# Performance work log

Measured on AMD Instinct MI355X. Metric: run time of the kernel, lower is better.

Reference implementation:

```python
import jax, jax.numpy as jnp
import numpy as np

N = 150000   # nodes
E = 150000   # edges per edge type
D = 128      # n_map
T = 10       # edge types: pre0-3, suc0-3, left, right
L = 4        # fuse layers
VOCAB = 16   # mark_type_dim
EPS = 1e-5


def _mlp(x, W1, b1, W2, b2):
    # MLPLayer(in, hid, out): Linear -> ReLU -> Linear
    return jax.nn.relu(x @ W1.T + b1) @ W2.T + b2


def setup_inputs() -> dict:
    key = jax.random.key(0)
    ks = iter(jax.random.split(key, 40))
    s = 0.02
    f = lambda shape: (jax.random.normal(next(ks), shape, dtype=jnp.float32) * s)
    inp = {
        'ctrs': jax.random.normal(next(ks), (N, 2), dtype=jnp.float32),
        'feats': jax.random.normal(next(ks), (N, 2), dtype=jnp.float32),
        # input MLP (2 -> D -> D)
        'in_W1': f((D, 2)), 'in_b1': f((D,)), 'in_W2': f((D, D)), 'in_b2': f((D,)),
        # seg MLP (2 -> D -> D)
        'seg_W1': f((D, 2)), 'seg_b1': f((D,)), 'seg_W2': f((D, D)), 'seg_b2': f((D,)),
        # mark embedding and meta MLP (2D -> D -> D)
        'embed': f((VOCAB, D)),
        'meta_W1': f((D, 2 * D)), 'meta_b1': f((D,)), 'meta_W2': f((D, D)), 'meta_b2': f((D,)),
        # fuse weights stacked over L layers
        'ctr_W': f((L, D, D)),            # Linear no bias
        'edge_W': f((L, T, D, D)),        # per-edge-type Linear no bias
        'norm_g': jnp.ones((L, D), jnp.float32),
        'norm_b': jnp.zeros((L, D), jnp.float32),
        'ctr2_W1': f((L, D, D)), 'ctr2_b1': f((L, D)),
        'ctr2_W2': f((L, D, D)), 'ctr2_b2': f((L, D)),
        # integer graph structure
        'mark_type': jax.random.randint(next(ks), (N,), 0, VOCAB, dtype=jnp.int32),
        'edge_u': jax.random.randint(next(ks), (T, E), 0, N, dtype=jnp.int32),
        'edge_v': jax.random.randint(next(ks), (T, E), 0, N, dtype=jnp.int32),
    }
    return inp


def reference(ctrs, feats, in_W1, in_b1, in_W2, in_b2,
              seg_W1, seg_b1, seg_W2, seg_b2,
              embed, meta_W1, meta_b1, meta_W2, meta_b2,
              ctr_W, edge_W, norm_g, norm_b,
              ctr2_W1, ctr2_b1, ctr2_W2, ctr2_b2,
              mark_type, edge_u, edge_v):
    feat = jax.nn.relu(_mlp(ctrs, in_W1, in_b1, in_W2, in_b2)
                       + _mlp(feats, seg_W1, seg_b1, seg_W2, seg_b2))  # [N, D]
    res = feat
    for i in range(L):
        temp = feat @ ctr_W[i].T
        for t in range(T):  # gather -> small GEMM -> scatter-add per edge type
            msg = feat[edge_v[t]] @ edge_W[i, t].T        # [E, D]
            temp = temp.at[edge_u[t]].add(msg)
        # GroupNorm(1, D) on [N, D]: normalize over channels per node
        mu = jnp.mean(temp, axis=-1, keepdims=True)
        var = jnp.var(temp, axis=-1, keepdims=True)
        feat = (temp - mu) * jax.lax.rsqrt(var + EPS) * norm_g[i] + norm_b[i]
        feat = jax.nn.relu(feat)
        feat = _mlp(feat, ctr2_W1[i], ctr2_b1[i], ctr2_W2[i], ctr2_b2[i])
        feat = jax.nn.relu(feat + res)
        res = feat
    meta = embed[mark_type]                               # [N, D]
    feat = _mlp(jnp.concatenate([feat, meta], axis=1), meta_W1, meta_b1, meta_W2, meta_b2)
    return feat
```

## Files before the change

### kernel.cpp

```cpp
#include <hip/hip_runtime.h>

#define D 128
#define NT 10
#define NL 4
#define BN 128
#define SCH 1024

typedef __attribute__((ext_vector_type(8))) short bf16x8;
typedef __attribute__((ext_vector_type(4))) float f32x4;

__device__ inline unsigned short f2bf(float x) {
    union { float f; unsigned u; } v; v.f = x;
    unsigned r = v.u + 0x7FFFu + ((v.u >> 16) & 1u);
    return (unsigned short)(r >> 16);
}
__device__ inline float bf2f(unsigned short h) {
    union { unsigned u; float f; } v; v.u = ((unsigned)h) << 16;
    return v.f;
}

__global__ void input_hidden_kernel(const float* __restrict__ ctrs,
                                    const float* __restrict__ feats,
                                    const float* __restrict__ inW1,
                                    const float* __restrict__ inb1,
                                    const float* __restrict__ segW1,
                                    const float* __restrict__ segb1,
                                    float* __restrict__ h_in,
                                    float* __restrict__ h_seg, int N) {
    int gid = blockIdx.x * blockDim.x + threadIdx.x;
    int n = gid >> 5;
    int c = gid & 31;
    if (n >= N) return;
    float x0 = ctrs[2 * n], x1 = ctrs[2 * n + 1];
    float y0 = feats[2 * n], y1 = feats[2 * n + 1];
    int o0 = c * 4;
    float hi[4], hs[4];
#pragma unroll
    for (int j = 0; j < 4; ++j) {
        int o = o0 + j;
        float a = fmaf(x0, inW1[2 * o], fmaf(x1, inW1[2 * o + 1], inb1[o]));
        hi[j] = fmaxf(a, 0.f);
        float b = fmaf(y0, segW1[2 * o], fmaf(y1, segW1[2 * o + 1], segb1[o]));
        hs[j] = fmaxf(b, 0.f);
    }
    *(float4*)&h_in[(size_t)n * D + o0] = make_float4(hi[0], hi[1], hi[2], hi[3]);
    *(float4*)&h_seg[(size_t)n * D + o0] = make_float4(hs[0], hs[1], hs[2], hs[3]);
}

template <int BIAS, int RELU, int ADDIN>
__global__ __launch_bounds__(256) void gemm_mfma_kernel(
    const float* __restrict__ A, const float* __restrict__ W,
    const float* __restrict__ bias, const float* addin, float* out, int N,
    int ldw) {
    __shared__ unsigned short a_hi[128][40], a_lo[128][40];
    __shared__ unsigned short w_hi[128][40], w_lo[128][40];
    int t = threadIdx.x;
    int wave = t >> 6, lane = t & 63;
    int fr = lane & 15, fq = lane >> 4;
    int n0 = blockIdx.x * BN;
    f32x4 acc[2][8];
#pragma unroll
    for (int m = 0; m < 2; ++m)
#pragma unroll
        for (int n = 0; n < 8; ++n) acc[m][n] = (f32x4){0.f, 0.f, 0.f, 0.f};

    for (int kc = 0; kc < 4; ++kc) {
        int k0 = kc * 32;
#pragma unroll
        for (int i = 0; i < 4; ++i) {
            int idx = i * 256 + t;
            int row = idx >> 3, c4 = idx & 7;
            int n = n0 + row;
            float4 v = make_float4(0.f, 0.f, 0.f, 0.f);
            if (n < N) v = *(const float4*)&A[(size_t)n * D + k0 + c4 * 4];
            ushort4 h, l;
            h.x = f2bf(v.x); l.x = f2bf(v.x - bf2f(h.x));
            h.y = f2bf(v.y); l.y = f2bf(v.y - bf2f(h.y));
            h.z = f2bf(v.z); l.z = f2bf(v.z - bf2f(h.z));
            h.w = f2bf(v.w); l.w = f2bf(v.w - bf2f(h.w));
            *(ushort4*)&a_hi[row][c4 * 4] = h;
            *(ushort4*)&a_lo[row][c4 * 4] = l;
        }
#pragma unroll
        for (int i = 0; i < 4; ++i) {
            int idx = i * 256 + t;
            int row = idx >> 3, c4 = idx & 7;
            float4 v = *(const float4*)&W[(size_t)row * ldw + k0 + c4 * 4];
            ushort4 h, l;
            h.x = f2bf(v.x); l.x = f2bf(v.x - bf2f(h.x));
            h.y = f2bf(v.y); l.y = f2bf(v.y - bf2f(h.y));
            h.z = f2bf(v.z); l.z = f2bf(v.z - bf2f(h.z));
            h.w = f2bf(v.w); l.w = f2bf(v.w - bf2f(h.w));
            *(ushort4*)&w_hi[row][c4 * 4] = h;
            *(ushort4*)&w_lo[row][c4 * 4] = l;
        }
        __syncthreads();

        bf16x8 ah[2], al[2];
#pragma unroll
        for (int m = 0; m < 2; ++m) {
            int row = wave * 32 + m * 16 + fr;
            ah[m] = *(const bf16x8*)&a_hi[row][fq * 8];
            al[m] = *(const bf16x8*)&a_lo[row][fq * 8];
        }
#pragma unroll
        for (int n = 0; n < 8; ++n) {
            int wr = n * 16 + fr;
            bf16x8 wh = *(const bf16x8*)&w_hi[wr][fq * 8];
            bf16x8 wl = *(const bf16x8*)&w_lo[wr][fq * 8];
#pragma unroll
            for (int m = 0; m < 2; ++m) {
                acc[m][n] = __builtin_amdgcn_mfma_f32_16x16x32_bf16(
                    ah[m], wh, acc[m][n], 0, 0, 0);
                acc[m][n] = __builtin_amdgcn_mfma_f32_16x16x32_bf16(
                    ah[m], wl, acc[m][n], 0, 0, 0);
                acc[m][n] = __builtin_amdgcn_mfma_f32_16x16x32_bf16(
                    al[m], wh, acc[m][n], 0, 0, 0);
            }
        }
        __syncthreads();
    }
#pragma unroll
    for (int m = 0; m < 2; ++m) {
#pragma unroll
        for (int j = 0; j < 4; ++j) {
            int row = n0 + wave * 32 + m * 16 + fq * 4 + j;
            if (row < N) {
#pragma unroll
                for (int n = 0; n < 8; ++n) {
                    int col = n * 16 + fr;
                    float r = acc[m][n][j];
                    if (BIAS) r += bias[col];
                    if (ADDIN) r += addin[(size_t)row * D + col];
                    if (RELU) r = fmaxf(r, 0.f);
                    out[(size_t)row * D + col] = r;
                }
            }
        }
    }
}

__global__ void csr_hist_kernel(const int* __restrict__ edge_u, int* deg,
                                int N, int E) {
    int gid = blockIdx.x * blockDim.x + threadIdx.x;
    if (gid >= NT * E) return;
    int t = gid / E;
    int u = edge_u[gid];
    atomicAdd(&deg[(size_t)t * N + u], 1);
}

__global__ __launch_bounds__(256) void csr_chunksum_kernel(
    const int* __restrict__ deg, int* csum, int N, int nch) {
    int b = blockIdx.x;
    int t = b / nch, ch = b % nch;
    int tid = threadIdx.x;
    const int* dg = deg + (size_t)t * N;
    int base = ch * SCH + tid * 4;
    int s = 0;
#pragma unroll
    for (int j = 0; j < 4; ++j) {
        int idx = base + j;
        if (idx < N) s += dg[idx];
    }
#pragma unroll
    for (int off = 32; off; off >>= 1) s += __shfl_down(s, off);
    __shared__ int wsum[4];
    if ((tid & 63) == 0) wsum[tid >> 6] = s;
    __syncthreads();
    if (tid == 0) csum[b] = wsum[0] + wsum[1] + wsum[2] + wsum[3];
}

__global__ void csr_chunkscan_kernel(int* csum, int* rowptr, int N, int nch) {
    int t = threadIdx.x;
    if (t >= NT) return;
    int run = 0;
    for (int i = 0; i < nch; ++i) {
        int v = csum[t * nch + i];
        csum[t * nch + i] = run;
        run += v;
    }
    rowptr[(size_t)t * (N + 1) + N] = run;
}

__global__ __launch_bounds__(256) void csr_blockscan_kernel(
    const int* __restrict__ deg, const int* __restrict__ csum, int* rowptr,
    int* cur, int N, int nch) {
    int b = blockIdx.x;
    int t = b / nch, ch = b % nch;
    int tid = threadIdx.x;
    const int* dg = deg + (size_t)t * N;
    int base = ch * SCH + tid * 4;
    int d[4];
    int s = 0;
#pragma unroll
    for (int j = 0; j < 4; ++j) {
        int idx = base + j;
        d[j] = (idx < N) ? dg[idx] : 0;
        s += d[j];
    }
    __shared__ int ps[256];
    ps[tid] = s;
    __syncthreads();
    for (int off = 1; off < 256; off <<= 1) {
        int v = (tid >= off) ? ps[tid - off] : 0;
        __syncthreads();
        ps[tid] += v;
        __syncthreads();
    }
    int excl = (tid ? ps[tid - 1] : 0) + csum[b];
    size_t rb = (size_t)t * (N + 1);
#pragma unroll
    for (int j = 0; j < 4; ++j) {
        int idx = base + j;
        if (idx < N) {
            rowptr[rb + idx] = excl;
            cur[rb + idx] = excl;
            excl += d[j];
        }
    }
}

__global__ void csr_fill_kernel(const int* __restrict__ edge_u,
                                const int* __restrict__ edge_v, int* cur,
                                int* col, int N, int E) {
    int gid = blockIdx.x * blockDim.x + threadIdx.x;
    if (gid >= NT * E) return;
    int t = gid / E;
    int u = edge_u[gid];
    int v = edge_v[gid];
    int pos = atomicAdd(&cur[(size_t)t * (N + 1) + u], 1);
    col[(size_t)t * E + pos] = v;
}

template <int NORM>
__global__ __launch_bounds__(256) void csr_gather_multi_kernel(
    const float* __restrict__ Y, const int* __restrict__ rowptr,
    const int* __restrict__ col, float* temp, int N, int nt, size_t strideY,
    int E, const float* __restrict__ g, const float* __restrict__ b) {
    int wid = (int)((blockIdx.x * (size_t)blockDim.x + threadIdx.x) >> 6);
    int lane = threadIdx.x & 63;
    if (wid >= N) return;
    size_t ro = (size_t)wid * D + lane * 2;
    float2 acc = *(float2*)&temp[ro];
    for (int j = 0; j < nt; ++j) {
        const int* rp = rowptr + (size_t)j * (N + 1);
        int beg = rp[wid];
        int end = rp[wid + 1];
        const float* Yj = Y + (size_t)j * strideY;
        const int* cj = col + (size_t)j * E;
        for (int k = beg; k < end; ++k) {
            int v = cj[k];
            float2 y = *(const float2*)&Yj[(size_t)v * D + lane * 2];
            acc.x += y.x;
            acc.y += y.y;
        }
    }
    if (NORM) {
        float s = acc.x + acc.y;
        float sq = acc.x * acc.x + acc.y * acc.y;
#pragma unroll
        for (int off = 32; off; off >>= 1) {
            s += __shfl_xor(s, off);
            sq += __shfl_xor(sq, off);
        }
        float mu = s * (1.f / 128.f);
        float var = sq * (1.f / 128.f) - mu * mu;
        float rs = rsqrtf(var + 1e-5f);
        acc.x = fmaxf(fmaf((acc.x - mu) * rs, g[lane * 2], b[lane * 2]), 0.f);
        acc.y = fmaxf(fmaf((acc.y - mu) * rs, g[lane * 2 + 1], b[lane * 2 + 1]), 0.f);
    }
    *(float2*)&temp[ro] = acc;
}

__global__ __launch_bounds__(256) void norm_relu_kernel(float* temp,
                                                        const float* __restrict__ g,
                                                        const float* __restrict__ b,
                                                        int N) {
    int wid = (int)((blockIdx.x * (size_t)blockDim.x + threadIdx.x) >> 6);
    int lane = threadIdx.x & 63;
    if (wid >= N) return;
    float2 x = *(float2*)&temp[(size_t)wid * D + lane * 2];
    float s = x.x + x.y;
    float sq = x.x * x.x + x.y * x.y;
#pragma unroll
    for (int off = 32; off; off >>= 1) {
        s += __shfl_xor(s, off);
        sq += __shfl_xor(sq, off);
    }
    float mu = s * (1.f / 128.f);
    float var = sq * (1.f / 128.f) - mu * mu;
    float rs = rsqrtf(var + 1e-5f);
    float r0 = fmaxf(fmaf((x.x - mu) * rs, g[lane * 2], b[lane * 2]), 0.f);
    float r1 = fmaxf(fmaf((x.y - mu) * rs, g[lane * 2 + 1], b[lane * 2 + 1]), 0.f);
    *(float2*)&temp[(size_t)wid * D + lane * 2] = make_float2(r0, r1);
}

__global__ void gather_meta_kernel(const int* __restrict__ mark,
                                   const float* __restrict__ embed, float* out,
                                   int N) {
    int gid = blockIdx.x * blockDim.x + threadIdx.x;
    int n = gid >> 5;
    int c = gid & 31;
    if (n >= N) return;
    *(float4*)&out[(size_t)n * D + c * 4] =
        *(const float4*)&embed[(size_t)mark[n] * D + c * 4];
}

static inline void launch_gemm(const float* A, const float* W, const float* bias,
                               const float* addin, float* out, int N, int ldw,
                               bool relu, hipStream_t s) {
    dim3 grid((N + BN - 1) / BN), blk(256);
    bool B = bias != nullptr, AD = addin != nullptr;
    if (B && !relu && !AD)
        gemm_mfma_kernel<1, 0, 0><<<grid, blk, 0, s>>>(A, W, bias, addin, out, N, ldw);
    else if (B && relu && AD)
        gemm_mfma_kernel<1, 1, 1><<<grid, blk, 0, s>>>(A, W, bias, addin, out, N, ldw);
    else if (!B && !relu && !AD)
        gemm_mfma_kernel<0, 0, 0><<<grid, blk, 0, s>>>(A, W, bias, addin, out, N, ldw);
    else if (B && relu && !AD)
        gemm_mfma_kernel<1, 1, 0><<<grid, blk, 0, s>>>(A, W, bias, addin, out, N, ldw);
    else if (!B && relu && AD)
        gemm_mfma_kernel<0, 1, 1><<<grid, blk, 0, s>>>(A, W, bias, addin, out, N, ldw);
    else if (!B && relu && !AD)
        gemm_mfma_kernel<0, 1, 0><<<grid, blk, 0, s>>>(A, W, bias, addin, out, N, ldw);
    else if (!B && !relu && AD)
        gemm_mfma_kernel<0, 0, 1><<<grid, blk, 0, s>>>(A, W, bias, addin, out, N, ldw);
    else
        gemm_mfma_kernel<1, 0, 1><<<grid, blk, 0, s>>>(A, W, bias, addin, out, N, ldw);
}

extern "C" void kernel_launch(void* const* d_in, const int* in_sizes, int n_in,
                              void* d_out, int out_size, void* d_ws,
                              size_t ws_size, hipStream_t stream) {
    const float* ctrs = (const float*)d_in[0];
    const float* feats = (const float*)d_in[1];
    const float* in_W1 = (const float*)d_in[2];
    const float* in_b1 = (const float*)d_in[3];
    const float* in_W2 = (const float*)d_in[4];
    const float* in_b2 = (const float*)d_in[5];
    const float* seg_W1 = (const float*)d_in[6];
    const float* seg_b1 = (const float*)d_in[7];
    const float* seg_W2 = (const float*)d_in[8];
    const float* seg_b2 = (const float*)d_in[9];
    const float* embed = (const float*)d_in[10];
    const float* meta_W1 = (const float*)d_in[11];
    const float* meta_b1 = (const float*)d_in[12];
    const float* meta_W2 = (const float*)d_in[13];
    const float* meta_b2 = (const float*)d_in[14];
    const float* ctr_W = (const float*)d_in[15];
    const float* edge_W = (const float*)d_in[16];
    const float* norm_g = (const float*)d_in[17];
    const float* norm_b = (const float*)d_in[18];
    const float* ctr2_W1 = (const float*)d_in[19];
    const float* ctr2_b1 = (const float*)d_in[20];
    const float* ctr2_W2 = (const float*)d_in[21];
    const float* ctr2_b2 = (const float*)d_in[22];
    const int* mark_type = (const int*)d_in[23];
    const int* edge_u = (const int*)d_in[24];
    const int* edge_v = (const int*)d_in[25];

    const int N = in_sizes[0] / 2;
    const int E = in_sizes[24] / NT;
    const size_t ND = (size_t)N * D;
    const int nch = (N + SCH - 1) / SCH;

    float* F = (float*)d_ws;
    float* T1 = (float*)d_ws + ND;
    float* SC = (float*)d_out;

    int* rowptr = (int*)((float*)d_ws + 2 * ND);
    int* col = rowptr + (size_t)NT * (N + 1);
    size_t base_ws = (2 * ND) * sizeof(float) +
                     ((size_t)NT * (N + 1) + (size_t)NT * E) * sizeof(int);
    size_t out_need = ((size_t)NT * N + (size_t)NT * (N + 1) +
                       2 * (size_t)NT * nch) * sizeof(int);
    bool use_csr = (ws_size >= base_ws) &&
                   ((size_t)out_size * sizeof(float) >= out_need);

    float* Yws = (float*)((char*)d_ws + ((base_ws + 255) & ~(size_t)255));
    int slots = 0;
    if (use_csr && ws_size > base_ws + 256)
        slots = (int)((ws_size - base_ws - 256) / (ND * sizeof(float)));
    if (slots > NT) slots = NT;

    dim3 blk(256);
    dim3 g32((N * 32 + 255) / 256);
    dim3 g64(((size_t)N * 64 + 255) / 256);
    dim3 gTE(((size_t)NT * E + 255) / 256);

    if (use_csr) {
        int* deg = (int*)d_out;
        int* cur = deg + (size_t)NT * N;
        int* csum = cur + (size_t)NT * (N + 1);
        hipMemsetAsync(deg, 0, (size_t)NT * N * sizeof(int), stream);
        csr_hist_kernel<<<gTE, blk, 0, stream>>>(edge_u, deg, N, E);
        csr_chunksum_kernel<<<NT * nch, blk, 0, stream>>>(deg, csum, N, nch);
        csr_chunkscan_kernel<<<1, 64, 0, stream>>>(csum, rowptr, N, nch);
        csr_blockscan_kernel<<<NT * nch, blk, 0, stream>>>(deg, csum, rowptr,
                                                           cur, N, nch);
        csr_fill_kernel<<<gTE, blk, 0, stream>>>(edge_u, edge_v, cur, col, N, E);
    }

    input_hidden_kernel<<<g32, blk, 0, stream>>>(ctrs, feats, in_W1, in_b1,
                                                 seg_W1, seg_b1, T1, SC, N);
    launch_gemm(T1, in_W2, in_b2, nullptr, F, N, D, false, stream);
    launch_gemm(SC, seg_W2, seg_b2, F, F, N, D, true, stream);

    for (int i = 0; i < NL; ++i) {
        launch_gemm(F, ctr_W + (size_t)i * D * D, nullptr, nullptr, T1, N, D,
                    false, stream);
        if (use_csr && slots >= 1) {
            int ngroups = (NT + slots - 1) / slots;
            for (int g0 = 0, grp = 0; g0 < NT; g0 += slots, ++grp) {
                int nt = (NT - g0 < slots) ? (NT - g0) : slots;
                for (int j = 0; j < nt; ++j)
                    launch_gemm(F, edge_W + ((size_t)i * NT + g0 + j) * D * D,
                                nullptr, nullptr, Yws + (size_t)j * ND, N, D,
                                false, stream);
                bool last = (grp == ngroups - 1);
                if (last && ngroups == 1)
                    csr_gather_multi_kernel<1><<<g64, blk, 0, stream>>>(
                        Yws, rowptr + (size_t)g0 * (N + 1), col + (size_t)g0 * E,
                        T1, N, nt, ND, E, norm_g + (size_t)i * D,
                        norm_b + (size_t)i * D);
                else
                    csr_gather_multi_kernel<0><<<g64, blk, 0, stream>>>(
                        Yws, rowptr + (size_t)g0 * (N + 1), col + (size_t)g0 * E,
                        T1, N, nt, ND, E, nullptr, nullptr);
            }
            if (ngroups > 1)
                norm_relu_kernel<<<g64, blk, 0, stream>>>(
                    T1, norm_g + (size_t)i * D, norm_b + (size_t)i * D, N);
        } else {
            for (int t = 0; t < NT; ++t) {
                launch_gemm(F, edge_W + ((size_t)i * NT + t) * D * D, nullptr,
                            nullptr, SC, N, D, false, stream);
                csr_gather_multi_kernel<0><<<g64, blk, 0, stream>>>(
                    SC, rowptr + (size_t)t * (N + 1), col + (size_t)t * E, T1,
                    N, 1, 0, E, nullptr, nullptr);
            }
            norm_relu_kernel<<<g64, blk, 0, stream>>>(
                T1, norm_g + (size_t)i * D, norm_b + (size_t)i * D, N);
        }
        launch_gemm(T1, ctr2_W1 + (size_t)i * D * D, ctr2_b1 + (size_t)i * D,
                    nullptr, SC, N, D, true, stream);
        launch_gemm(SC, ctr2_W2 + (size_t)i * D * D, ctr2_b2 + (size_t)i * D, F,
                    F, N, D, true, stream);
    }

    gather_meta_kernel<<<g32, blk, 0, stream>>>(mark_type, embed, SC, N);
    launch_gemm(F, meta_W1, meta_b1, nullptr, T1, N, 2 * D, false, stream);
    launch_gemm(SC, meta_W1 + D, nullptr, T1, T1, N, 2 * D, true, stream);
    launch_gemm(T1, meta_W2, meta_b2, nullptr, (float*)d_out, N, D, false,
                stream);
}
```

Before: 4.722 ms.

## Preconvert weights to split bf16 once and stream multi-output GEMM over activation tile

Adds a one-time kernel that converts all 57 weight matrices to hi/lo bf16 pairs, so the GEMMs no longer redo that conversion per block. The GEMM now loads activations straight from global memory into registers with no LDS staging or barriers, and it can loop over up to 11 weight matrices per row tile. This lets one launch produce the ctr_W result and all ten edge-type results while reusing the A fragments. It also reorganises workspace buffers and drops the separate norm kernel. The cost is that weight fragments come uncached-in-LDS from global/L2 and register pressure rises.

```diff
diff --git a/kernel.cpp b/kernel.cpp
--- a/kernel.cpp
+++ b/kernel.cpp
@@ -3,11 +3,15 @@
 #define D 128
 #define NT 10
 #define NL 4
-#define BN 128
 #define SCH 1024
+#define NMAT 57
+#define MATSZ 32768
 
 typedef __attribute__((ext_vector_type(8))) short bf16x8;
 typedef __attribute__((ext_vector_type(4))) float f32x4;
+
+struct OutPtrs { float* p[11]; };
+struct CvtTab { const float* src[NMAT]; int ldw[NMAT]; };
 
 __device__ inline unsigned short f2bf(float x) {
     union { float f; unsigned u; } v; v.f = x;
@@ -17,6 +21,36 @@
 __device__ inline float bf2f(unsigned short h) {
     union { unsigned u; float f; } v; v.u = ((unsigned)h) << 16;
     return v.f;
+}
+
+__device__ inline void cvt8(const float4& v0, const float4& v1, bf16x8& h,
+                            bf16x8& l) {
+    float f[8] = {v0.x, v0.y, v0.z, v0.w, v1.x, v1.y, v1.z, v1.w};
+#pragma unroll
+    for (int j = 0; j < 8; ++j) {
+        unsigned short hh = f2bf(f[j]);
+        h[j] = (short)hh;
+        l[j] = (short)f2bf(f[j] - bf2f(hh));
+    }
+}
+
+__global__ __launch_bounds__(256) void wcvt_kernel(CvtTab tab,
+                                                   unsigned short* dst) {
+    int bid = blockIdx.x;
+    int mat = bid >> 4;
+    if (mat >= NMAT) return;
+    int e = (bid & 15) * 1024 + threadIdx.x * 4;
+    int o = e >> 7, k = e & 127;
+    const float* s = tab.src[mat];
+    int ldw = tab.ldw[mat];
+    float4 v = *(const float4*)&s[(size_t)o * ldw + k];
+    ushort4 h, l;
+    h.x = f2bf(v.x); l.x = f2bf(v.x - bf2f(h.x));
+    h.y = f2bf(v.y); l.y = f2bf(v.y - bf2f(h.y));
+    h.z = f2bf(v.z); l.z = f2bf(v.z - bf2f(h.z));
+    h.w = f2bf(v.w); l.w = f2bf(v.w - bf2f(h.w));
+    *(ushort4*)&dst[(size_t)mat * MATSZ + e] = h;
+    *(ushort4*)&dst[(size_t)mat * MATSZ + 16384 + e] = l;
 }
 
 __global__ void input_hidden_kernel(const float* __restrict__ ctrs,
@@ -48,92 +82,74 @@
 }
 
 template <int BIAS, int RELU, int ADDIN>
-__global__ __launch_bounds__(256) void gemm_mfma_kernel(
-    const float* __restrict__ A, const float* __restrict__ W,
-    const float* __restrict__ bias, const float* addin, float* out, int N,
-    int ldw) {
-    __shared__ unsigned short a_hi[128][40], a_lo[128][40];
-    __shared__ unsigned short w_hi[128][40], w_lo[128][40];
+__global__ __launch_bounds__(256) void gemm_stream_kernel(
+    const float* __restrict__ A, const unsigned short* __restrict__ Wc,
+    int nw, OutPtrs outs, const float* __restrict__ bias,
+    const float* __restrict__ addin, int N) {
     int t = threadIdx.x;
     int wave = t >> 6, lane = t & 63;
     int fr = lane & 15, fq = lane >> 4;
-    int n0 = blockIdx.x * BN;
-    f32x4 acc[2][8];
-#pragma unroll
-    for (int m = 0; m < 2; ++m)
-#pragma unroll
-        for (int n = 0; n < 8; ++n) acc[m][n] = (f32x4){0.f, 0.f, 0.f, 0.f};
-
-    for (int kc = 0; kc < 4; ++kc) {
-        int k0 = kc * 32;
-#pragma unroll
-        for (int i = 0; i < 4; ++i) {
-            int idx = i * 256 + t;
-            int row = idx >> 3, c4 = idx & 7;
-            int n = n0 + row;
-            float4 v = make_float4(0.f, 0.f, 0.f, 0.f);
-            if (n < N) v = *(const float4*)&A[(size_t)n * D + k0 + c4 * 4];
-            ushort4 h, l;
-            h.x = f2bf(v.x); l.x = f2bf(v.x - bf2f(h.x));
-            h.y = f2bf(v.y); l.y = f2bf(v.y - bf2f(h.y));
-            h.z = f2bf(v.z); l.z = f2bf(v.z - bf2f(h.z));
-            h.w = f2bf(v.w); l.w = f2bf(v.w - bf2f(h.w));
-            *(ushort4*)&a_hi[row][c4 * 4] = h;
-            *(ushort4*)&a_lo[row][c4 * 4] = l;
-        }
-#pragma unroll
-        for (int i = 0; i < 4; ++i) {
-            int idx = i * 256 + t;
-            int row = idx >> 3, c4 = idx & 7;
-            float4 v = *(const float4*)&W[(size_t)row * ldw + k0 + c4 * 4];
-            ushort4 h, l;
-            h.x = f2bf(v.x); l.x = f2bf(v.x - bf2f(h.x));
-            h.y = f2bf(v.y); l.y = f2bf(v.y - bf2f(h.y));
-            h.z = f2bf(v.z); l.z = f2bf(v.z - bf2f(h.z));
-            h.w = f2bf(v.w); l.w = f2bf(v.w - bf2f(h.w));
-            *(ushort4*)&w_hi[row][c4 * 4] = h;
-            *(ushort4*)&w_lo[row][c4 * 4] = l;
-        }
-        __syncthreads();
-
-        bf16x8 ah[2], al[2];
+    int rbase = blockIdx.x * 128 + wave * 32;
+    int r0 = rbase + fr, r1 = rbase + 16 + fr;
+    bool ok0 = r0 < N, ok1 = r1 < N;
+    const float* a0 = A + (size_t)r0 * D;
+    const float* a1 = A + (size_t)r1 * D;
+
+    for (int w = 0; w < nw; ++w) {
+        const unsigned short* wm = Wc + (size_t)w * MATSZ;
+        f32x4 acc[2][8];
+#pragma unroll
+        for (int m = 0; m < 2; ++m)
+#pragma unroll
+            for (int n = 0; n < 8; ++n) acc[m][n] = (f32x4){0.f, 0.f, 0.f, 0.f};
+
+#pragma unroll
+        for (int kc = 0; kc < 4; ++kc) {
+            int ko = kc * 32 + fq * 8;
+            bf16x8 ah0, al0, ah1, al1;
+            {
+                float4 v0 = {0.f, 0.f, 0.f, 0.f}, v1 = {0.f, 0.f, 0.f, 0.f};
+                if (ok0) {
+                    v0 = *(const float4*)(a0 + ko);
+                    v1 = *(const float4*)(a0 + ko + 4);
+                }
+                cvt8(v0, v1, ah0, al0);
+                float4 u0 = {0.f, 0.f, 0.f, 0.f}, u1 = {0.f, 0.f, 0.f, 0.f};
+                if (ok1) {
+                    u0 = *(const float4*)(a1 + ko);
+                    u1 = *(const float4*)(a1 + ko + 4);
+                }
+                cvt8(u0, u1, ah1, al1);
+            }
+#pragma unroll
+            for (int n = 0; n < 8; ++n) {
+                const unsigned short* wp = wm + (size_t)(n * 16 + fr) * D + ko;
+                bf16x8 wh = *(const bf16x8*)wp;
+                bf16x8 wl = *(const bf16x8*)(wp + 16384);
+                acc[0][n] = __builtin_amdgcn_mfma_f32_16x16x32_bf16(ah0, wh, acc[0][n], 0, 0, 0);
+                acc[0][n] = __builtin_amdgcn_mfma_f32_16x16x32_bf16(ah0, wl, acc[0][n], 0, 0, 0);
+                acc[0][n] = __builtin_amdgcn_mfma_f32_16x16x32_bf16(al0, wh, acc[0][n], 0, 0, 0);
+                acc[1][n] = __builtin_amdgcn_mfma_f32_16x16x32_bf16(ah1, wh, acc[1][n], 0, 0, 0);
+                acc[1][n] = __builtin_amdgcn_mfma_f32_16x16x32_bf16(ah1, wl, acc[1][n], 0, 0, 0);
+                acc[1][n] = __builtin_amdgcn_mfma_f32_16x16x32_bf16(al1, wh, acc[1][n], 0, 0, 0);
+            }
+        }
+        float* outp = outs.p[w];
 #pragma unroll
         for (int m = 0; m < 2; ++m) {
-            int row = wave * 32 + m * 16 + fr;
-            ah[m] = *(const bf16x8*)&a_hi[row][fq * 8];
-            al[m] = *(const bf16x8*)&a_lo[row][fq * 8];
-        }
-#pragma unroll
-        for (int n = 0; n < 8; ++n) {
-            int wr = n * 16 + fr;
-            bf16x8 wh = *(const bf16x8*)&w_hi[wr][fq * 8];
-            bf16x8 wl = *(const bf16x8*)&w_lo[wr][fq * 8];
-#pragma unroll
-            for (int m = 0; m < 2; ++m) {
-                acc[m][n] = __builtin_amdgcn_mfma_f32_16x16x32_bf16(
-                    ah[m], wh, acc[m][n], 0, 0, 0);
-                acc[m][n] = __builtin_amdgcn_mfma_f32_16x16x32_bf16(
-                    ah[m], wl, acc[m][n], 0, 0, 0);
-                acc[m][n] = __builtin_amdgcn_mfma_f32_16x16x32_bf16(
-                    al[m], wh, acc[m][n], 0, 0, 0);
-            }
-        }
-        __syncthreads();
-    }
-#pragma unroll
-    for (int m = 0; m < 2; ++m) {
-#pragma unroll
-        for (int j = 0; j < 4; ++j) {
-            int row = n0 + wave * 32 + m * 16 + fq * 4 + j;
-            if (row < N) {
-#pragma unroll
-                for (int n = 0; n < 8; ++n) {
-                    int col = n * 16 + fr;
-                    float r = acc[m][n][j];
-                    if (BIAS) r += bias[col];
-                    if (ADDIN) r += addin[(size_t)row * D + col];
-                    if (RELU) r = fmaxf(r, 0.f);
-                    out[(size_t)row * D + col] = r;
+#pragma unroll
+            for (int j = 0; j < 4; ++j) {
+                int row = rbase + m * 16 + fq * 4 + j;
+                if (row < N) {
+#pragma unroll
+                    for (int n = 0; n < 8; ++n) {
+                        int colx = n * 16 + fr;
+                        float r = acc[m][n][j];
+                        if (BIAS) r += bias[colx];
+                        if (ADDIN) r += addin[(size_t)row * D + colx];
+                        if (RELU) r = fmaxf(r, 0.f);
+                        outp[(size_t)row * D + colx] = r;
+                    }
                 }
             }
         }
@@ -272,29 +288,6 @@
     *(float2*)&temp[ro] = acc;
 }
 
-__global__ __launch_bounds__(256) void norm_relu_kernel(float* temp,
-                                                        const float* __restrict__ g,
-                                                        const float* __restrict__ b,
-                                                        int N) {
-    int wid = (int)((blockIdx.x * (size_t)blockDim.x + threadIdx.x) >> 6);
-    int lane = threadIdx.x & 63;
-    if (wid >= N) return;
-    float2 x = *(float2*)&temp[(size_t)wid * D + lane * 2];
-    float s = x.x + x.y;
-    float sq = x.x * x.x + x.y * x.y;
-#pragma unroll
-    for (int off = 32; off; off >>= 1) {
-        s += __shfl_xor(s, off);
-        sq += __shfl_xor(sq, off);
-    }
-    float mu = s * (1.f / 128.f);
-    float var = sq * (1.f / 128.f) - mu * mu;
-    float rs = rsqrtf(var + 1e-5f);
-    float r0 = fmaxf(fmaf((x.x - mu) * rs, g[lane * 2], b[lane * 2]), 0.f);
-    float r1 = fmaxf(fmaf((x.y - mu) * rs, g[lane * 2 + 1], b[lane * 2 + 1]), 0.f);
-    *(float2*)&temp[(size_t)wid * D + lane * 2] = make_float2(r0, r1);
-}
-
 __global__ void gather_meta_kernel(const int* __restrict__ mark,
                                    const float* __restrict__ embed, float* out,
                                    int N) {
@@ -306,27 +299,29 @@
         *(const float4*)&embed[(size_t)mark[n] * D + c * 4];
 }
 
-static inline void launch_gemm(const float* A, const float* W, const float* bias,
-                               const float* addin, float* out, int N, int ldw,
-                               bool relu, hipStream_t s) {
-    dim3 grid((N + BN - 1) / BN), blk(256);
+static inline void launch_gemm1(const float* A, const unsigned short* Wc,
+                                const float* bias, const float* addin,
+                                float* out, int N, bool relu, hipStream_t s) {
+    OutPtrs o{};
+    o.p[0] = out;
+    dim3 grid((N + 127) / 128), blk(256);
     bool B = bias != nullptr, AD = addin != nullptr;
     if (B && !relu && !AD)
-        gemm_mfma_kernel<1, 0, 0><<<grid, blk, 0, s>>>(A, W, bias, addin, out, N, ldw);
+        gemm_stream_kernel<1, 0, 0><<<grid, blk, 0, s>>>(A, Wc, 1, o, bias, addin, N);
     else if (B && relu && AD)
-        gemm_mfma_kernel<1, 1, 1><<<grid, blk, 0, s>>>(A, W, bias, addin, out, N, ldw);
-    else if (!B && !relu && !AD)
-        gemm_mfma_kernel<0, 0, 0><<<grid, blk, 0, s>>>(A, W, bias, addin, out, N, ldw);
+        gemm_stream_kernel<1, 1, 1><<<grid, blk, 0, s>>>(A, Wc, 1, o, bias, addin, N);
     else if (B && relu && !AD)
-        gemm_mfma_kernel<1, 1, 0><<<grid, blk, 0, s>>>(A, W, bias, addin, out, N, ldw);
+        gemm_stream_kernel<1, 1, 0><<<grid, blk, 0, s>>>(A, Wc, 1, o, bias, addin, N);
+    else if (B && !relu && AD)
+        gemm_stream_kernel<1, 0, 1><<<grid, blk, 0, s>>>(A, Wc, 1, o, bias, addin, N);
     else if (!B && relu && AD)
-        gemm_mfma_kernel<0, 1, 1><<<grid, blk, 0, s>>>(A, W, bias, addin, out, N, ldw);
+        gemm_stream_kernel<0, 1, 1><<<grid, blk, 0, s>>>(A, Wc, 1, o, bias, addin, N);
     else if (!B && relu && !AD)
-        gemm_mfma_kernel<0, 1, 0><<<grid, blk, 0, s>>>(A, W, bias, addin, out, N, ldw);
+        gemm_stream_kernel<0, 1, 0><<<grid, blk, 0, s>>>(A, Wc, 1, o, bias, addin, N);
     else if (!B && !relu && AD)
-        gemm_mfma_kernel<0, 0, 1><<<grid, blk, 0, s>>>(A, W, bias, addin, out, N, ldw);
+        gemm_stream_kernel<0, 0, 1><<<grid, blk, 0, s>>>(A, Wc, 1, o, bias, addin, N);
     else
-        gemm_mfma_kernel<1, 0, 1><<<grid, blk, 0, s>>>(A, W, bias, addin, out, N, ldw);
+        gemm_stream_kernel<0, 0, 0><<<grid, blk, 0, s>>>(A, Wc, 1, o, bias, addin, N);
 }
 
 extern "C" void kernel_launch(void* const* d_in, const int* in_sizes, int n_in,
@@ -364,31 +359,47 @@
     const size_t ND = (size_t)N * D;
     const int nch = (N + SCH - 1) / SCH;
 
-    float* F = (float*)d_ws;
-    float* T1 = (float*)d_ws + ND;
+    unsigned short* Wcvt = (unsigned short*)d_ws;
+    size_t wcB = ((size_t)NMAT * MATSZ * sizeof(unsigned short) + 255) & ~(size_t)255;
+    float* F = (float*)((char*)d_ws + wcB);
+    int* rowptr = (int*)(F + ND);
+    int* col = rowptr + (size_t)NT * (N + 1);
+    size_t used = (size_t)((char*)(col + (size_t)NT * E) - (char*)d_ws);
+    used = (used + 255) & ~(size_t)255;
+    float* Yws = (float*)((char*)d_ws + used);
+    long navail = 0;
+    if (ws_size > used) navail = (long)((ws_size - used) / (ND * sizeof(float)));
+    if (navail > 11) navail = 11;
+    if (navail < 1) navail = 1;
+
     float* SC = (float*)d_out;
 
-    int* rowptr = (int*)((float*)d_ws + 2 * ND);
-    int* col = rowptr + (size_t)NT * (N + 1);
-    size_t base_ws = (2 * ND) * sizeof(float) +
-                     ((size_t)NT * (N + 1) + (size_t)NT * E) * sizeof(int);
-    size_t out_need = ((size_t)NT * N + (size_t)NT * (N + 1) +
-                       2 * (size_t)NT * nch) * sizeof(int);
-    bool use_csr = (ws_size >= base_ws) &&
-                   ((size_t)out_size * sizeof(float) >= out_need);
-
-    float* Yws = (float*)((char*)d_ws + ((base_ws + 255) & ~(size_t)255));
-    int slots = 0;
-    if (use_csr && ws_size > base_ws + 256)
-        slots = (int)((ws_size - base_ws - 256) / (ND * sizeof(float)));
-    if (slots > NT) slots = NT;
+    CvtTab tab;
+    tab.src[0] = in_W2;  tab.ldw[0] = D;
+    tab.src[1] = seg_W2; tab.ldw[1] = D;
+    for (int i = 0; i < NL; ++i) { tab.src[2 + i] = ctr2_W1 + (size_t)i * D * D; tab.ldw[2 + i] = D; }
+    for (int i = 0; i < NL; ++i) { tab.src[6 + i] = ctr2_W2 + (size_t)i * D * D; tab.ldw[6 + i] = D; }
+    for (int i = 0; i < NL; ++i) {
+        for (int t = 0; t < NT; ++t) {
+            int id = 10 + i * 11 + t;
+            tab.src[id] = edge_W + ((size_t)i * NT + t) * D * D;
+            tab.ldw[id] = D;
+        }
+        int id = 10 + i * 11 + 10;
+        tab.src[id] = ctr_W + (size_t)i * D * D;
+        tab.ldw[id] = D;
+    }
+    tab.src[54] = meta_W1;     tab.ldw[54] = 2 * D;
+    tab.src[55] = meta_W1 + D; tab.ldw[55] = 2 * D;
+    tab.src[56] = meta_W2;     tab.ldw[56] = D;
+    wcvt_kernel<<<NMAT * 16, 256, 0, stream>>>(tab, Wcvt);
 
     dim3 blk(256);
     dim3 g32((N * 32 + 255) / 256);
     dim3 g64(((size_t)N * 64 + 255) / 256);
     dim3 gTE(((size_t)NT * E + 255) / 256);
 
-    if (use_csr) {
+    {
         int* deg = (int*)d_out;
         int* cur = deg + (size_t)NT * N;
         int* csum = cur + (size_t)NT * (N + 1);
@@ -396,61 +407,84 @@
         csr_hist_kernel<<<gTE, blk, 0, stream>>>(edge_u, deg, N, E);
         csr_chunksum_kernel<<<NT * nch, blk, 0, stream>>>(deg, csum, N, nch);
         csr_chunkscan_kernel<<<1, 64, 0, stream>>>(csum, rowptr, N, nch);
-        csr_blockscan_kernel<<<NT * nch, blk, 0, stream>>>(deg, csum, rowptr,
-                                                           cur, N, nch);
+        csr_blockscan_kernel<<<NT * nch, blk, 0, stream>>>(deg, csum, rowptr, cur, N, nch);
         csr_fill_kernel<<<gTE, blk, 0, stream>>>(edge_u, edge_v, cur, col, N, E);
     }
 
-    input_hidden_kernel<<<g32, blk, 0, stream>>>(ctrs, feats, in_W1, in_b1,
-                                                 seg_W1, seg_b1, T1, SC, N);
-    launch_gemm(T1, in_W2, in_b2, nullptr, F, N, D, false, stream);
-    launch_gemm(SC, seg_W2, seg_b2, F, F, N, D, true, stream);
+    bool slotted = navail >= 2;
+    int gs = slotted ? (int)navail - 1 : 0;
+    if (gs > NT) gs = NT;
+    float* temp = slotted ? Yws + (size_t)gs * ND : Yws;
+    float* h2buf = (slotted && gs >= 2) ? Yws + ND : (slotted ? temp : SC);
+
+    {
+        float* h1 = slotted ? Yws : temp;
+        float* h2 = slotted ? h2buf : SC;
+        input_hidden_kernel<<<g32, blk, 0, stream>>>(ctrs, feats, in_W1, in_b1,
+                                                     seg_W1, seg_b1, h1, h2, N);
+        launch_gemm1(h1, Wcvt + (size_t)0 * MATSZ, in_b2, nullptr, F, N, false, stream);
+        launch_gemm1(h2, Wcvt + (size_t)1 * MATSZ, seg_b2, F, F, N, true, stream);
+    }
 
     for (int i = 0; i < NL; ++i) {
-        launch_gemm(F, ctr_W + (size_t)i * D * D, nullptr, nullptr, T1, N, D,
-                    false, stream);
-        if (use_csr && slots >= 1) {
-            int ngroups = (NT + slots - 1) / slots;
-            for (int g0 = 0, grp = 0; g0 < NT; g0 += slots, ++grp) {
-                int nt = (NT - g0 < slots) ? (NT - g0) : slots;
-                for (int j = 0; j < nt; ++j)
-                    launch_gemm(F, edge_W + ((size_t)i * NT + g0 + j) * D * D,
-                                nullptr, nullptr, Yws + (size_t)j * ND, N, D,
-                                false, stream);
-                bool last = (grp == ngroups - 1);
-                if (last && ngroups == 1)
+        const unsigned short* layerW = Wcvt + (size_t)(10 + i * 11) * MATSZ;
+        if (slotted && gs == NT) {
+            OutPtrs o;
+            for (int j = 0; j < NT; ++j) o.p[j] = Yws + (size_t)j * ND;
+            o.p[10] = temp;
+            gemm_stream_kernel<0, 0, 0><<<dim3((N + 127) / 128), blk, 0, stream>>>(
+                F, layerW, 11, o, nullptr, nullptr, N);
+            csr_gather_multi_kernel<1><<<g64, blk, 0, stream>>>(
+                Yws, rowptr, col, temp, N, NT, ND, E, norm_g + (size_t)i * D,
+                norm_b + (size_t)i * D);
+        } else if (slotted) {
+            launch_gemm1(F, layerW + (size_t)10 * MATSZ, nullptr, nullptr, temp, N, false, stream);
+            for (int g0 = 0; g0 < NT; g0 += gs) {
+                int cnt = (NT - g0 < gs) ? (NT - g0) : gs;
+                OutPtrs o;
+                for (int j = 0; j < cnt; ++j) o.p[j] = Yws + (size_t)j * ND;
+                gemm_stream_kernel<0, 0, 0><<<dim3((N + 127) / 128), blk, 0, stream>>>(
+                    F, layerW + (size_t)g0 * MATSZ, cnt, o, nullptr, nullptr, N);
+                bool last = (g0 + cnt == NT);
+                if (last)
                     csr_gather_multi_kernel<1><<<g64, blk, 0, stream>>>(
                         Yws, rowptr + (size_t)g0 * (N + 1), col + (size_t)g0 * E,
-                        T1, N, nt, ND, E, norm_g + (size_t)i * D,
+                        temp, N, cnt, ND, E, norm_g + (size_t)i * D,
                         norm_b + (size_t)i * D);
                 else
                     csr_gather_multi_kernel<0><<<g64, blk, 0, stream>>>(
                         Yws, rowptr + (size_t)g0 * (N + 1), col + (size_t)g0 * E,
-                        T1, N, nt, ND, E, nullptr, nullptr);
+                        temp, N, cnt, ND, E, nullptr, nullptr);
             }
-            if (ngroups > 1)
-                norm_relu_kernel<<<g64, blk, 0, stream>>>(
-                    T1, norm_g + (size_t)i * D, norm_b + (size_t)i * D, N);
         } else {
+            launch_gemm1(F, layerW + (size_t)10 * MATSZ, nullptr, nullptr, temp, N, false, stream);
             for (int t = 0; t < NT; ++t) {
-                launch_gemm(F, edge_W + ((size_t)i * NT + t) * D * D, nullptr,
-                            nullptr, SC, N, D, false, stream);
-                csr_gather_multi_kernel<0><<<g64, blk, 0, stream>>>(
-                    SC, rowptr + (size_t)t * (N + 1), col + (size_t)t * E, T1,
-                    N, 1, 0, E, nullptr, nullptr);
+                launch_gemm1(F, layerW + (size_t)t * MATSZ, nullptr, nullptr, SC, N, false, stream);
+                bool last = (t == NT - 1);
+                if (last)
+                    csr_gather_multi_kernel<1><<<g64, blk, 0, stream>>>(
+                        SC, rowptr + (size_t)t * (N + 1), col + (size_t)t * E,
+                        temp, N, 1, ND, E, norm_g + (size_t)i * D,
+                        norm_b + (size_t)i * D);
+                else
+                    csr_gather_multi_kernel<0><<<g64, blk, 0, stream>>>(
+                        SC, rowptr + (size_t)t * (N + 1), col + (size_t)t * E,
+                        temp, N, 1, ND, E, nullptr, nullptr);
             }
-            norm_relu_kernel<<<g64, blk, 0, stream>>>(
-                T1, norm_g + (size_t)i * D, norm_b + (size_t)i * D, N);
-        }
-        launch_gemm(T1, ctr2_W1 + (size_t)i * D * D, ctr2_b1 + (size_t)i * D,
-                    nullptr, SC, N, D, true, stream);
-        launch_gemm(SC, ctr2_W2 + (size_t)i * D * D, ctr2_b2 + (size_t)i * D, F,
-                    F, N, D, true, stream);
-    }
-
-    gather_meta_kernel<<<g32, blk, 0, stream>>>(mark_type, embed, SC, N);
-    launch_gemm(F, meta_W1, meta_b1, nullptr, T1, N, 2 * D, false, stream);
-    launch_gemm(SC, meta_W1 + D, nullptr, T1, T1, N, 2 * D, true, stream);
-    launch_gemm(T1, meta_W2, meta_b2, nullptr, (float*)d_out, N, D, false,
-                stream);
-}
+        }
+        float* H = slotted ? Yws : SC;
+        launch_gemm1(temp, Wcvt + (size_t)(2 + i) * MATSZ, ctr2_b1 + (size_t)i * D,
+                     nullptr, H, N, true, stream);
+        launch_gemm1(H, Wcvt + (size_t)(6 + i) * MATSZ, ctr2_b2 + (size_t)i * D,
+                     F, F, N, true, stream);
+    }
+
+    {
+        float* M = slotted ? Yws : SC;
+        float* H = slotted ? h2buf : temp;
+        gather_meta_kernel<<<g32, blk, 0, stream>>>(mark_type, embed, M, N);
+        launch_gemm1(F, Wcvt + (size_t)54 * MATSZ, meta_b1, nullptr, H, N, false, stream);
+        launch_gemm1(M, Wcvt + (size_t)55 * MATSZ, nullptr, H, H, N, true, stream);
+        launch_gemm1(H, Wcvt + (size_t)56 * MATSZ, meta_b2, nullptr, (float*)d_out, N, false, stream);
+    }
+}
```

Result: slower. 5.522 ms (+16.9%).
